# Kernel tuning notes

Hardware: AMD Instinct MI355X
Metric: run time of the kernel (lower is better)

## Reference

```python
import jax, jax.numpy as jnp
import numpy as np

CUTOFF = 5.0
NUM_RBF = 8
POLY_P = 5
AVG_NEIGH = 16.0
NUM_LAYERS = 2
NUM_RANKS = 4  # edge angular ranks 0..3 (Cartesian dims 1,3,9,27)
C = 64


def _radial(edge_vec):
    # r: [E,1]; Bessel-j0 basis with polynomial cutoff envelope (MACE-style)
    r = jnp.sqrt(jnp.sum(edge_vec * edge_vec, axis=-1, keepdims=True) + 1e-12)
    x = r / CUTOFF
    p = float(POLY_P)
    env = (1.0 - 0.5 * (p + 1.0) * (p + 2.0) * x**POLY_P
           + p * (p + 2.0) * x**(POLY_P + 1)
           - 0.5 * p * (p + 1.0) * x**(POLY_P + 2))
    env = jnp.where(x < 1.0, env, 0.0)
    k = jnp.arange(1, NUM_RBF + 1, dtype=edge_vec.dtype)
    basis = jnp.sqrt(2.0 / CUTOFF) * jnp.sin(k * jnp.pi * x) / r  # [E,K]
    return basis * env, r


def _angular(rhat):
    # Cartesian ICTD-style angular basis, ranks 0..3, norm constants sqrt(2r+1)
    E = rhat.shape[0]
    y0 = jnp.ones((E, 1), rhat.dtype)
    y1 = jnp.sqrt(3.0) * rhat  # [E,3]
    o2 = rhat[:, :, None] * rhat[:, None, :]
    y2 = jnp.sqrt(5.0) * o2.reshape(E, 9)
    o3 = o2[:, :, :, None] * rhat[:, None, None, :]
    y3 = jnp.sqrt(7.0) * o3.reshape(E, 27)
    return (y0, y1, y2, y3)


def setup_inputs() -> dict:
    key = jax.random.key(0)
    ks = jax.random.split(key, 12)
    N, E = 5000, 80000
    species = jax.random.randint(ks[0], (N,), 0, 10, dtype=jnp.int32)
    senders = jax.random.randint(ks[1], (E,), 0, N, dtype=jnp.int32)
    receivers = jax.random.randint(ks[2], (E,), 0, N, dtype=jnp.int32)
    edge_vec = 1.5 * jax.random.normal(ks[3], (E, 3), jnp.float32)
    embed_w = jax.random.normal(ks[4], (10, C), jnp.float32)
    rad_w1 = jax.random.normal(ks[5], (NUM_LAYERS, NUM_RBF, 64), jnp.float32) / np.sqrt(NUM_RBF)
    rad_w2 = jax.random.normal(ks[6], (NUM_LAYERS, 64, 64), jnp.float32) / 8.0
    rad_w3 = jax.random.normal(ks[7], (NUM_LAYERS, 64, 64), jnp.float32) / 8.0
    rad_w4 = jax.random.normal(ks[8], (NUM_LAYERS, 64, NUM_RANKS * C), jnp.float32) / 8.0
    mix_w = jax.random.normal(ks[9], (NUM_LAYERS, NUM_RANKS, C, C), jnp.float32) / 8.0
    read_w = jax.random.normal(ks[10], (NUM_LAYERS, C), jnp.float32) / 8.0
    return {"species": species, "senders": senders, "receivers": receivers,
            "edge_vec": edge_vec, "embed_w": embed_w, "rad_w1": rad_w1,
            "rad_w2": rad_w2, "rad_w3": rad_w3, "rad_w4": rad_w4,
            "mix_w": mix_w, "read_w": read_w}


def reference(species, senders, receivers, edge_vec, embed_w,
              rad_w1, rad_w2, rad_w3, rad_w4, mix_w, read_w):
    N = species.shape[0]
    E = edge_vec.shape[0]
    rb, r = _radial(edge_vec)                      # [E,K]
    rhat = edge_vec / r
    Y = _angular(rhat)                             # tuple of [E,dim_r]
    h0 = embed_w[species]                          # [N,C] species embedding
    node_energy = jnp.zeros((N,), edge_vec.dtype)
    for l in range(NUM_LAYERS):
        # radial MLP -> per-rank, per-channel edge weights [E, NUM_RANKS, C]
        h = jax.nn.silu(rb @ rad_w1[l])
        h = jax.nn.silu(h @ rad_w2[l])
        h = jax.nn.silu(h @ rad_w3[l])
        R = (h @ rad_w4[l]).reshape(E, NUM_RANKS, C)
        hj = h0[senders]                           # neighbor gather [E,C]
        h0_new = jnp.zeros_like(h0)
        for ri in range(NUM_RANKS):
            # equivariant edge tensor product: radial * scalar feat x angular
            m = (R[:, ri, :] * hj)[:, :, None] * Y[ri][:, None, :]  # [E,C,dim]
            A = jax.ops.segment_sum(m, receivers, num_segments=N) / AVG_NEIGH
            if ri == 0:
                h0_new = h0_new + A[..., 0] @ mix_w[l, 0]
            else:
                # correlation-2 invariant contraction of equivariant features
                h0_new = h0_new + jnp.einsum('ncd,ncd->nc', A, A) @ mix_w[l, ri]
        node_energy = node_energy + h0_new @ read_w[l]
        h0 = h0_new
    return node_energy
```

## Files before the change

kernel.cpp:

```cpp
#include <hip/hip_runtime.h>
#include <math.h>


#define PI_F 3.14159265358979323846f
#define LOG2E_F 1.44269504088896340736f

typedef _Float16 f16x8 __attribute__((ext_vector_type(8)));
typedef float f32x4 __attribute__((ext_vector_type(4)));

union FU { uint4 u; f16x8 h; };

__device__ __forceinline__ float silu_f(float x) {
    float e = __builtin_amdgcn_exp2f(-LOG2E_F * x);
    return x * __builtin_amdgcn_rcpf(1.0f + e);
}

__device__ __forceinline__ uint pack2_f16(float a, float b) {
    return __builtin_bit_cast(uint, __builtin_amdgcn_cvt_pkrtz(a, b));
}

__device__ __forceinline__ float unpk_f16(uint u, int hi) {
    unsigned short s = hi ? (unsigned short)(u >> 16) : (unsigned short)(u & 0xffff);
    return (float)__builtin_bit_cast(_Float16, s);
}

__global__ void k_setup(const float* __restrict__ rw1,
                        const float* __restrict__ rw2,
                        const float* __restrict__ rw3,
                        const float* __restrict__ rw4,
                        uint* __restrict__ Wf1, uint* __restrict__ Wf2,
                        uint* __restrict__ Wf3, uint* __restrict__ Wf4,
                        const int* __restrict__ species,
                        const float* __restrict__ embw,
                        float* __restrict__ h0,
                        int* __restrict__ counts, int* __restrict__ cursor,
                        int N, int NC)
{
    int tid = blockIdx.x * blockDim.x + threadIdx.x;
    if (tid < N) { counts[tid] = 0; cursor[tid] = 0; }
    if (tid < NC) {
        int n = tid >> 6, c = tid & 63;
        h0[tid] = embw[species[n]*64 + c];
    }
    if (tid < 2048) {
        int reg = tid & 3, lane = (tid >> 2) & 63, ot = (tid >> 8) & 3, l = tid >> 10;
        int out = 16*ot + (lane & 15);
        int k   = 8*(lane >> 4) + 2*reg;
        float lo = (k   < 8) ? rw1[l*512 + k*64 + out]     : 0.0f;
        float hi = (k+1 < 8) ? rw1[l*512 + (k+1)*64 + out] : 0.0f;
        Wf1[tid] = pack2_f16(lo, hi);
    }
    if (tid >= 2048 && tid < 2048 + 4096) {
        int t = tid - 2048;
        int reg = t & 3, lane = (t >> 2) & 63, kt = (t >> 8) & 1, ot = (t >> 9) & 3, l = t >> 11;
        int out = 16*ot + (lane & 15);
        int k   = 32*kt + 8*(lane >> 4) + 2*reg;
        Wf2[t] = pack2_f16(rw2[l*4096 + k*64 + out], rw2[l*4096 + (k+1)*64 + out]);
    }
    if (tid >= 6144 && tid < 6144 + 4096) {
        int t = tid - 6144;
        int reg = t & 3, lane = (t >> 2) & 63, kt = (t >> 8) & 1, ot = (t >> 9) & 3, l = t >> 11;
        int out = 16*ot + (lane & 15);
        int k   = 32*kt + 8*(lane >> 4) + 2*reg;
        Wf3[t] = pack2_f16(rw3[l*4096 + k*64 + out], rw3[l*4096 + (k+1)*64 + out]);
    }
    if (tid >= 10240 && tid < 10240 + 16384) {
        int t = tid - 10240;
        int reg = t & 3, lane = (t >> 2) & 63, kt = (t >> 8) & 1, ot = (t >> 9) & 15, l = t >> 13;
        int out = 16*ot + (lane & 15);
        int k   = 32*kt + 8*(lane >> 4) + 2*reg;
        Wf4[t] = pack2_f16(rw4[l*16384 + k*256 + out], rw4[l*16384 + (k+1)*256 + out]);
    }
}

__global__ void k_edge_basis(const float* __restrict__ ev,
                             const int* __restrict__ recv,
                             uint*  __restrict__ rbh,
                             float* __restrict__ rhat4,
                             int*   __restrict__ counts,
                             int E)
{
    int e = blockIdx.x * blockDim.x + threadIdx.x;
    if (e >= E) return;
    float vx = ev[3*e+0], vy = ev[3*e+1], vz = ev[3*e+2];
    float r2 = vx*vx + vy*vy + vz*vz + 1e-12f;
    float r  = sqrtf(r2);
    float x  = r * 0.2f;
    float x2 = x*x;
    float x5 = x2*x2*x;
    float env = 1.0f + x5*(-21.0f + x*(35.0f - 15.0f*x));
    if (x >= 1.0f) env = 0.0f;
    float pref = 0.632455532033675866f / r * env;
    float pix  = PI_F * x;
    float bas[8];
    #pragma unroll
    for (int k = 0; k < 8; ++k) bas[k] = pref * __sinf((float)(k+1) * pix);
    uint* o = rbh + (size_t)e*4;
    #pragma unroll
    for (int k = 0; k < 4; ++k) o[k] = pack2_f16(bas[2*k], bas[2*k+1]);

    float ir = 1.0f / r;
    float4 rh;
    rh.x = vx*ir; rh.y = vy*ir; rh.z = vz*ir; rh.w = 0.0f;
    *(float4*)(rhat4 + (size_t)e*4) = rh;

    atomicAdd(&counts[recv[e]], 1);
}

__global__ void k_scan(const int* __restrict__ counts, int* __restrict__ offsets, int N)
{
    __shared__ int wsum[16];
    __shared__ int basev;
    int lane = threadIdx.x & 63;
    int w    = threadIdx.x >> 6;
    if (threadIdx.x == 0) basev = 0;
    __syncthreads();
    for (int start = 0; start < N; start += 1024) {
        int i = start + (int)threadIdx.x;
        int v = (i < N) ? counts[i] : 0;
        int s = v;
        #pragma unroll
        for (int off = 1; off < 64; off <<= 1) {
            int t = __shfl_up(s, off, 64);
            if (lane >= off) s += t;
        }
        if (lane == 63) wsum[w] = s;
        __syncthreads();
        int wbase = 0;
        {
            int ws = (lane < 16) ? wsum[lane] : 0;
            #pragma unroll
            for (int off = 1; off < 16; off <<= 1) {
                int t = __shfl_up(ws, off, 64);
                if (lane >= off) ws += t;
            }
            int excl = __shfl(ws, w - 1, 64);
            wbase = (w == 0) ? 0 : excl;
        }
        if (i < N) offsets[i] = basev + wbase + s - v;
        __syncthreads();
        if (threadIdx.x == 1023) basev += wbase + s;
        __syncthreads();
    }
    if (threadIdx.x == 0) offsets[N] = basev;
}

__global__ void k_scatter(const int* __restrict__ recv,
                          const int* __restrict__ offsets,
                          int* __restrict__ cursor,
                          int* __restrict__ elist, int E)
{
    int e = blockIdx.x * blockDim.x + threadIdx.x;
    if (e >= E) return;
    int r = recv[e];
    int p = atomicAdd(&cursor[r], 1);
    elist[offsets[r] + p] = e;
}

__global__ __launch_bounds__(256) void k_sort_wave(
    const int* __restrict__ offsets, int* __restrict__ elist, int N)
{
    int lane = threadIdx.x & 63;
    int node = (blockIdx.x * blockDim.x + threadIdx.x) >> 6;
    if (node >= N) return;
    int beg = offsets[node], end = offsets[node+1];
    int d = end - beg;
    if (d <= 1) return;
    if (d <= 64) {
        int v = (lane < d) ? elist[beg + lane] : 0x7fffffff;
        int rank = 0;
        #pragma unroll 8
        for (int j = 0; j < 64; ++j) {
            int vj = __shfl(v, j, 64);
            rank += (vj < v) ? 1 : 0;
        }
        if (lane < d) elist[beg + rank] = v;
    } else {
        if (lane == 0) {
            for (int i = beg + 1; i < end; ++i) {
                int v = elist[i];
                int j = i - 1;
                while (j >= beg && elist[j] > v) { elist[j+1] = elist[j]; --j; }
                elist[j+1] = v;
            }
        }
    }
}

__global__ void k_permute(const int* __restrict__ elist,
                          const int* __restrict__ senders,
                          const float* __restrict__ rhat4,
                          int* __restrict__ eslot,
                          int* __restrict__ csr_send,
                          float* __restrict__ csr_rhat,
                          int E)
{
    int s = blockIdx.x * blockDim.x + threadIdx.x;
    if (s >= E) return;
    int e = elist[s];
    eslot[e] = s;
    csr_send[s] = senders[e];
    *(float4*)(csr_rhat + (size_t)s*4) = *(const float4*)(rhat4 + (size_t)e*4);
}

__global__ __launch_bounds__(256) void k_mlp_mfma(
    const uint* __restrict__ rbh,
    const uint* __restrict__ Wf1, const uint* __restrict__ Wf2,
    const uint* __restrict__ Wf3, const uint* __restrict__ Wf4,
    const int* __restrict__ eslot,
    uint* __restrict__ Rpk,
    int E, int tiles)
{
    __shared__ __align__(16) uint Hl[4][16][132];
    int lane = threadIdx.x & 63;
    int w    = threadIdx.x >> 6;
    int wid  = blockIdx.x * 4 + w;
    if (wid >= 2 * tiles) return;
    int l    = wid / tiles;
    int tile = wid % tiles;
    int e0   = tile * 16;

    uint (*H)[132] = Hl[w];
    int er = lane & 15;
    int kb = lane >> 4;

    f32x4 zero4 = {0.f, 0.f, 0.f, 0.f};

    FU b;
    if (kb == 0) {
        int e = e0 + er;
        if (e < E) b.u = *(const uint4*)(rbh + (size_t)e*4);
        else       b.u = make_uint4(0,0,0,0);
    } else {
        b.u = make_uint4(0,0,0,0);
    }
    f32x4 d[4];
    #pragma unroll
    for (int ot = 0; ot < 4; ++ot) {
        FU a;
        a.u = *(const uint4*)(Wf1 + ((size_t)(l*4 + ot)*64 + lane)*4);
        d[ot] = __builtin_amdgcn_mfma_f32_16x16x32_f16(a.h, b.h, zero4, 0, 0, 0);
    }
    #pragma unroll
    for (int ot = 0; ot < 4; ++ot) {
        uint p0 = pack2_f16(silu_f(d[ot][0]), silu_f(d[ot][1]));
        uint p1 = pack2_f16(silu_f(d[ot][2]), silu_f(d[ot][3]));
        uint* dst = &H[er][8*ot + 2*kb];
        dst[0] = p0; dst[1] = p1;
    }

    const uint* Wfs[2] = { Wf2, Wf3 };
    #pragma unroll
    for (int s = 0; s < 2; ++s) {
        FU hb0, hb1;
        hb0.u = *(const uint4*)&H[er][4*kb];
        hb1.u = *(const uint4*)&H[er][16 + 4*kb];
        #pragma unroll
        for (int ot = 0; ot < 4; ++ot) {
            FU a;
            a.u = *(const uint4*)(Wfs[s] + ((size_t)((l*4 + ot)*2 + 0)*64 + lane)*4);
            d[ot] = __builtin_amdgcn_mfma_f32_16x16x32_f16(a.h, hb0.h, zero4, 0, 0, 0);
            a.u = *(const uint4*)(Wfs[s] + ((size_t)((l*4 + ot)*2 + 1)*64 + lane)*4);
            d[ot] = __builtin_amdgcn_mfma_f32_16x16x32_f16(a.h, hb1.h, d[ot], 0, 0, 0);
        }
        #pragma unroll
        for (int ot = 0; ot < 4; ++ot) {
            uint p0 = pack2_f16(silu_f(d[ot][0]), silu_f(d[ot][1]));
            uint p1 = pack2_f16(silu_f(d[ot][2]), silu_f(d[ot][3]));
            uint* dst = &H[er][8*ot + 2*kb];
            dst[0] = p0; dst[1] = p1;
        }
    }

    FU hb0, hb1;
    hb0.u = *(const uint4*)&H[er][4*kb];
    hb1.u = *(const uint4*)&H[er][16 + 4*kb];
    #pragma unroll
    for (int ri = 0; ri < 4; ++ri) {
        #pragma unroll
        for (int otl = 0; otl < 4; ++otl) {
            int ot = ri*4 + otl;
            FU a;
            f32x4 d2;
            a.u = *(const uint4*)(Wf4 + ((size_t)((l*16 + ot)*2 + 0)*64 + lane)*4);
            d2 = __builtin_amdgcn_mfma_f32_16x16x32_f16(a.h, hb0.h, zero4, 0, 0, 0);
            a.u = *(const uint4*)(Wf4 + ((size_t)((l*16 + ot)*2 + 1)*64 + lane)*4);
            d2 = __builtin_amdgcn_mfma_f32_16x16x32_f16(a.h, hb1.h, d2, 0, 0, 0);
            int p = otl*8 + kb*2;
            H[er][(p  )*4 + ri] = pack2_f16(d2[0], d2[1]);
            H[er][(p+1)*4 + ri] = pack2_f16(d2[2], d2[3]);
        }
    }
    #pragma unroll
    for (int it = 0; it < 8; ++it) {
        int f   = it*64 + lane;
        int row = f >> 5;
        int q4  = (f & 31) * 4;
        int eg  = e0 + row;
        if (eg < E) {
            int slot = eslot[eg];
            *(uint4*)(Rpk + ((size_t)l*E + slot)*128 + q4) = *(const uint4*)&H[row][q4];
        }
    }
}

__global__ __launch_bounds__(256) void k_node(
    const uint*  __restrict__ Rpk,
    const float* __restrict__ h0,
    const int*   __restrict__ csr_send,
    const float* __restrict__ csr_rhat,
    const int*   __restrict__ offsets,
    const float* __restrict__ mixw,
    const float* __restrict__ readw,
    float* __restrict__ h0n,
    const float* __restrict__ eprev,
    float* __restrict__ eout,
    int N)
{
    int gtid = blockIdx.x * blockDim.x + threadIdx.x;
    int wave = gtid >> 6;
    int lane = threadIdx.x & 63;
    int w    = threadIdx.x >> 6;
    __shared__ float Bl[4][4][64];
    bool active = (wave < N);
    int n = active ? wave : 0;
    int half  = lane & 1;
    int cpair = lane >> 1;

    float a0 = 0.f;
    float a1[3]  = {0.f,0.f,0.f};
    float a2[6]  = {0.f,0.f,0.f,0.f,0.f,0.f};
    float a3[10] = {0.f,0.f,0.f,0.f,0.f,0.f,0.f,0.f,0.f,0.f};

    auto accum = [&](float x, float y, float z, float hj, uint4 qv) {
        float t0 = unpk_f16(qv.x, half) * hj;
        float t1 = unpk_f16(qv.y, half) * hj;
        float t2 = unpk_f16(qv.z, half) * hj;
        float t3 = unpk_f16(qv.w, half) * hj;
        a0 += t0;
        a1[0] = fmaf(t1, x, a1[0]);
        a1[1] = fmaf(t1, y, a1[1]);
        a1[2] = fmaf(t1, z, a1[2]);
        float qxx = x*x, qxy = x*y, qxz = x*z, qyy = y*y, qyz = y*z, qzz = z*z;
        a2[0] = fmaf(t2, qxx, a2[0]);
        a2[1] = fmaf(t2, qxy, a2[1]);
        a2[2] = fmaf(t2, qxz, a2[2]);
        a2[3] = fmaf(t2, qyy, a2[3]);
        a2[4] = fmaf(t2, qyz, a2[4]);
        a2[5] = fmaf(t2, qzz, a2[5]);
        float u0 = t3*qxx, u1 = t3*qxy, u3 = t3*qyy, u5 = t3*qzz;
        a3[0] = fmaf(u0, x, a3[0]);
        a3[1] = fmaf(u0, y, a3[1]);
        a3[2] = fmaf(u0, z, a3[2]);
        a3[3] = fmaf(u3, x, a3[3]);
        a3[4] = fmaf(u1, z, a3[4]);
        a3[5] = fmaf(u5, x, a3[5]);
        a3[6] = fmaf(u3, y, a3[6]);
        a3[7] = fmaf(u3, z, a3[7]);
        a3[8] = fmaf(u5, y, a3[8]);
        a3[9] = fmaf(u5, z, a3[9]);
    };

    if (active) {
        int beg = __builtin_amdgcn_readfirstlane(offsets[n]);
        int end = __builtin_amdgcn_readfirstlane(offsets[n+1]);
        int i = beg;
        for (; i + 4 <= end; i += 4) {
            int sn_[4]; float4 rh_[4]; float hj_[4]; uint4 q_[4];
            #pragma unroll
            for (int k = 0; k < 4; ++k) sn_[k] = csr_send[i+k];
            #pragma unroll
            for (int k = 0; k < 4; ++k) {
                rh_[k] = *(const float4*)(csr_rhat + (size_t)(i+k)*4);
                q_[k]  = *(const uint4*)(Rpk + (size_t)(i+k)*128 + cpair*4);
            }
            #pragma unroll
            for (int k = 0; k < 4; ++k) hj_[k] = h0[(size_t)sn_[k]*64 + lane];
            #pragma unroll
            for (int k = 0; k < 4; ++k)
                accum(rh_[k].x, rh_[k].y, rh_[k].z, hj_[k], q_[k]);
        }
        for (; i < end; ++i) {
            int snd = csr_send[i];
            float4 rh = *(const float4*)(csr_rhat + (size_t)i*4);
            uint4  qv = *(const uint4*)(Rpk + (size_t)i*128 + cpair*4);
            float  hj = h0[(size_t)snd*64 + lane];
            accum(rh.x, rh.y, rh.z, hj, qv);
        }
    }

    float B0 = a0 * 0.0625f;
    float s1 = a1[0]*a1[0] + a1[1]*a1[1] + a1[2]*a1[2];
    float B1 = s1 * (3.0f/256.0f);
    float s2 = a2[0]*a2[0] + a2[3]*a2[3] + a2[5]*a2[5]
             + 2.0f*(a2[1]*a2[1] + a2[2]*a2[2] + a2[4]*a2[4]);
    float B2 = s2 * (5.0f/256.0f);
    float s3 = a3[0]*a3[0] + a3[6]*a3[6] + a3[9]*a3[9]
             + 3.0f*(a3[1]*a3[1] + a3[2]*a3[2] + a3[3]*a3[3]
                   + a3[5]*a3[5] + a3[7]*a3[7] + a3[8]*a3[8])
             + 6.0f*a3[4]*a3[4];
    float B3 = s3 * (7.0f/256.0f);

    Bl[w][0][lane] = B0;
    Bl[w][1][lane] = B1;
    Bl[w][2][lane] = B2;
    Bl[w][3][lane] = B3;
    __syncthreads();

    if (active) {
        float acc = 0.0f;
        for (int ri = 0; ri < 4; ++ri) {
            #pragma unroll 8
            for (int j = 0; j < 64; ++j)
                acc = fmaf(Bl[w][ri][j], mixw[(ri*64 + j)*64 + lane], acc);
        }
        h0n[(size_t)n*64 + lane] = acc;

        float evl = acc * readw[lane];
        #pragma unroll
        for (int off = 1; off < 64; off <<= 1) evl += __shfl_xor(evl, off, 64);
        if (lane == 0) {
            float o = evl;
            if (eprev) o += eprev[n];
            eout[n] = o;
        }
    }
}

extern "C" void kernel_launch(void* const* d_in, const int* in_sizes, int n_in,
                              void* d_out, int out_size, void* d_ws, size_t ws_size,
                              hipStream_t stream)
{
    const int*   species   = (const int*)  d_in[0];
    const int*   senders   = (const int*)  d_in[1];
    const int*   receivers = (const int*)  d_in[2];
    const float* edge_vec  = (const float*)d_in[3];
    const float* embed_w   = (const float*)d_in[4];
    const float* rad_w1    = (const float*)d_in[5];
    const float* rad_w2    = (const float*)d_in[6];
    const float* rad_w3    = (const float*)d_in[7];
    const float* rad_w4    = (const float*)d_in[8];
    const float* mix_w     = (const float*)d_in[9];
    const float* read_w    = (const float*)d_in[10];

    int N = in_sizes[0];
    int E = in_sizes[1];
    float* out = (float*)d_out;

    char* ws = (char*)d_ws;
    size_t off = 0;
    auto alloc = [&](size_t bytes) -> char* {
        char* p = ws + off;
        off = (off + bytes + 255) & ~(size_t)255;
        return p;
    };
    uint*  rbh     = (uint*) alloc((size_t)E*4*sizeof(uint));
    float* rhat4   = (float*)alloc((size_t)E*4*sizeof(float));
    float* h0a     = (float*)alloc((size_t)N*64*sizeof(float));
    float* h0b     = (float*)alloc((size_t)N*64*sizeof(float));
    float* ener    = (float*)alloc((size_t)N*sizeof(float));
    int* counts    = (int*)alloc((size_t)N*sizeof(int));
    int* offsets   = (int*)alloc((size_t)(N+1)*sizeof(int));
    int* cursor    = (int*)alloc((size_t)N*sizeof(int));
    int* elist     = (int*)alloc((size_t)E*sizeof(int));
    int* eslot     = (int*)alloc((size_t)E*sizeof(int));
    int* csr_send  = (int*)alloc((size_t)E*sizeof(int));
    float* csr_rhat= (float*)alloc((size_t)E*4*sizeof(float));
    uint* Wf1      = (uint*)alloc(2048*sizeof(uint));
    uint* Wf2      = (uint*)alloc(4096*sizeof(uint));
    uint* Wf3      = (uint*)alloc(4096*sizeof(uint));
    uint* Wf4      = (uint*)alloc(16384*sizeof(uint));
    uint* Rpk      = (uint*)alloc((size_t)2*E*128*sizeof(uint));

    int NC = N * 64;
    k_setup<<<(NC + 255)/256, 256, 0, stream>>>(
        rad_w1, rad_w2, rad_w3, rad_w4, Wf1, Wf2, Wf3, Wf4,
        species, embed_w, h0a, counts, cursor, N, NC);

    k_edge_basis<<<(E + 255)/256, 256, 0, stream>>>(
        edge_vec, receivers, rbh, rhat4, counts, E);
    k_scan<<<1, 1024, 0, stream>>>(counts, offsets, N);
    k_scatter<<<(E + 255)/256, 256, 0, stream>>>(receivers, offsets, cursor, elist, E);
    k_sort_wave<<<((size_t)N*64 + 255)/256, 256, 0, stream>>>(offsets, elist, N);
    k_permute<<<(E + 255)/256, 256, 0, stream>>>(
        elist, senders, rhat4, eslot, csr_send, csr_rhat, E);

    int tiles = (E + 15) / 16;
    int waves = 2 * tiles;
    k_mlp_mfma<<<(waves + 3)/4, 256, 0, stream>>>(
        rbh, Wf1, Wf2, Wf3, Wf4, eslot, Rpk, E, tiles);

    float* hcur = h0a;
    float* hnxt = h0b;
    for (int l = 0; l < 2; ++l) {
        uint* Rl = Rpk + (size_t)l * E * 128;
        k_node<<<((size_t)N*64 + 255)/256, 256, 0, stream>>>(
            Rl, hcur, csr_send, csr_rhat, offsets,
            mix_w + (size_t)l*4*64*64,
            read_w + (size_t)l*64,
            hnxt,
            (l == 0) ? nullptr : ener,
            (l == 0) ? ener : out,
            N);
        float* tmp = hcur; hcur = hnxt; hnxt = tmp;
    }
}
```

Baseline: 113.1 us.

## Fuse sort with permute and split node edge loop across wave pairs

Merges the per-node edge sort with the CSR permutation into one kernel, so the separate permute launch and its re-read of elist go away. The node kernel now gives each node two waves that each accumulate half of the edges. Partial accumulators are combined through shared memory, and the mix-weight contraction is split by rank between the two waves. This doubles the waves working on the gather-heavy edge loop to improve latency hiding, at the cost of extra shared-memory traffic and two more block barriers.

Result: no change. 114.4 us (+1.1%).

```diff
diff --git a/kernel.cpp b/kernel.cpp
--- a/kernel.cpp
+++ b/kernel.cpp
@@ -157,15 +157,22 @@
     elist[offsets[r] + p] = e;
 }
 
-__global__ __launch_bounds__(256) void k_sort_wave(
-    const int* __restrict__ offsets, int* __restrict__ elist, int N)
+__global__ __launch_bounds__(256) void k_sort_perm(
+    const int* __restrict__ offsets,
+    int* __restrict__ elist,
+    const int* __restrict__ senders,
+    const float* __restrict__ rhat4,
+    int* __restrict__ eslot,
+    int* __restrict__ csr_send,
+    float* __restrict__ csr_rhat,
+    int N)
 {
     int lane = threadIdx.x & 63;
     int node = (blockIdx.x * blockDim.x + threadIdx.x) >> 6;
     if (node >= N) return;
     int beg = offsets[node], end = offsets[node+1];
     int d = end - beg;
-    if (d <= 1) return;
+    if (d <= 0) return;
     if (d <= 64) {
         int v = (lane < d) ? elist[beg + lane] : 0x7fffffff;
         int rank = 0;
@@ -174,7 +181,12 @@
             int vj = __shfl(v, j, 64);
             rank += (vj < v) ? 1 : 0;
         }
-        if (lane < d) elist[beg + rank] = v;
+        if (lane < d) {
+            int slot = beg + rank;
+            eslot[v] = slot;
+            csr_send[slot] = senders[v];
+            *(float4*)(csr_rhat + (size_t)slot*4) = *(const float4*)(rhat4 + (size_t)v*4);
+        }
     } else {
         if (lane == 0) {
             for (int i = beg + 1; i < end; ++i) {
@@ -183,24 +195,14 @@
                 while (j >= beg && elist[j] > v) { elist[j+1] = elist[j]; --j; }
                 elist[j+1] = v;
             }
-        }
-    }
-}
-
-__global__ void k_permute(const int* __restrict__ elist,
-                          const int* __restrict__ senders,
-                          const float* __restrict__ rhat4,
-                          int* __restrict__ eslot,
-                          int* __restrict__ csr_send,
-                          float* __restrict__ csr_rhat,
-                          int E)
-{
-    int s = blockIdx.x * blockDim.x + threadIdx.x;
-    if (s >= E) return;
-    int e = elist[s];
-    eslot[e] = s;
-    csr_send[s] = senders[e];
-    *(float4*)(csr_rhat + (size_t)s*4) = *(const float4*)(rhat4 + (size_t)e*4);
+            for (int s = beg; s < end; ++s) {
+                int e = elist[s];
+                eslot[e] = s;
+                csr_send[s] = senders[e];
+                *(float4*)(csr_rhat + (size_t)s*4) = *(const float4*)(rhat4 + (size_t)e*4);
+            }
+        }
+    }
 }
 
 __global__ __launch_bounds__(256) void k_mlp_mfma(
@@ -317,13 +319,16 @@
     float* __restrict__ eout,
     int N)
 {
-    int gtid = blockIdx.x * blockDim.x + threadIdx.x;
-    int wave = gtid >> 6;
     int lane = threadIdx.x & 63;
     int w    = threadIdx.x >> 6;
-    __shared__ float Bl[4][4][64];
-    bool active = (wave < N);
-    int n = active ? wave : 0;
+    int pair = w >> 1;
+    int sub  = w & 1;
+    int n    = blockIdx.x * 2 + pair;
+    bool active = (n < N);
+
+    __shared__ float Bp[2][20][64];
+    __shared__ float Bl[2][4][64];
+
     int half  = lane & 1;
     int cpair = lane >> 1;
 
@@ -364,8 +369,13 @@
     if (active) {
         int beg = __builtin_amdgcn_readfirstlane(offsets[n]);
         int end = __builtin_amdgcn_readfirstlane(offsets[n+1]);
-        int i = beg;
-        for (; i + 4 <= end; i += 4) {
+        int cnt = end - beg;
+        int hsz = (cnt + 1) >> 1;
+        int b0  = beg + sub * hsz;
+        int b1  = sub ? end : (beg + hsz);
+
+        int i = b0;
+        for (; i + 4 <= b1; i += 4) {
             int sn_[4]; float4 rh_[4]; float hj_[4]; uint4 q_[4];
             #pragma unroll
             for (int k = 0; k < 4; ++k) sn_[k] = csr_send[i+k];
@@ -380,7 +390,7 @@
             for (int k = 0; k < 4; ++k)
                 accum(rh_[k].x, rh_[k].y, rh_[k].z, hj_[k], q_[k]);
         }
-        for (; i < end; ++i) {
+        for (; i < b1; ++i) {
             int snd = csr_send[i];
             float4 rh = *(const float4*)(csr_rhat + (size_t)i*4);
             uint4  qv = *(const uint4*)(Rpk + (size_t)i*128 + cpair*4);
@@ -389,31 +399,59 @@
         }
     }
 
-    float B0 = a0 * 0.0625f;
-    float s1 = a1[0]*a1[0] + a1[1]*a1[1] + a1[2]*a1[2];
-    float B1 = s1 * (3.0f/256.0f);
-    float s2 = a2[0]*a2[0] + a2[3]*a2[3] + a2[5]*a2[5]
-             + 2.0f*(a2[1]*a2[1] + a2[2]*a2[2] + a2[4]*a2[4]);
-    float B2 = s2 * (5.0f/256.0f);
-    float s3 = a3[0]*a3[0] + a3[6]*a3[6] + a3[9]*a3[9]
-             + 3.0f*(a3[1]*a3[1] + a3[2]*a3[2] + a3[3]*a3[3]
-                   + a3[5]*a3[5] + a3[7]*a3[7] + a3[8]*a3[8])
-             + 6.0f*a3[4]*a3[4];
-    float B3 = s3 * (7.0f/256.0f);
-
-    Bl[w][0][lane] = B0;
-    Bl[w][1][lane] = B1;
-    Bl[w][2][lane] = B2;
-    Bl[w][3][lane] = B3;
+    if (active && sub == 1) {
+        Bp[pair][0][lane] = a0;
+        #pragma unroll
+        for (int j = 0; j < 3; ++j)  Bp[pair][1+j][lane]  = a1[j];
+        #pragma unroll
+        for (int j = 0; j < 6; ++j)  Bp[pair][4+j][lane]  = a2[j];
+        #pragma unroll
+        for (int j = 0; j < 10; ++j) Bp[pair][10+j][lane] = a3[j];
+    }
     __syncthreads();
 
+    if (active && sub == 0) {
+        a0 += Bp[pair][0][lane];
+        #pragma unroll
+        for (int j = 0; j < 3; ++j)  a1[j] += Bp[pair][1+j][lane];
+        #pragma unroll
+        for (int j = 0; j < 6; ++j)  a2[j] += Bp[pair][4+j][lane];
+        #pragma unroll
+        for (int j = 0; j < 10; ++j) a3[j] += Bp[pair][10+j][lane];
+
+        float B0 = a0 * 0.0625f;
+        float s1 = a1[0]*a1[0] + a1[1]*a1[1] + a1[2]*a1[2];
+        float B1 = s1 * (3.0f/256.0f);
+        float s2 = a2[0]*a2[0] + a2[3]*a2[3] + a2[5]*a2[5]
+                 + 2.0f*(a2[1]*a2[1] + a2[2]*a2[2] + a2[4]*a2[4]);
+        float B2 = s2 * (5.0f/256.0f);
+        float s3 = a3[0]*a3[0] + a3[6]*a3[6] + a3[9]*a3[9]
+                 + 3.0f*(a3[1]*a3[1] + a3[2]*a3[2] + a3[3]*a3[3]
+                       + a3[5]*a3[5] + a3[7]*a3[7] + a3[8]*a3[8])
+                 + 6.0f*a3[4]*a3[4];
+        float B3 = s3 * (7.0f/256.0f);
+        Bl[pair][0][lane] = B0;
+        Bl[pair][1][lane] = B1;
+        Bl[pair][2][lane] = B2;
+        Bl[pair][3][lane] = B3;
+    }
+    __syncthreads();
+
+    float accw = 0.0f;
     if (active) {
-        float acc = 0.0f;
-        for (int ri = 0; ri < 4; ++ri) {
+        #pragma unroll
+        for (int rr = 0; rr < 2; ++rr) {
+            int ri = sub*2 + rr;
             #pragma unroll 8
             for (int j = 0; j < 64; ++j)
-                acc = fmaf(Bl[w][ri][j], mixw[(ri*64 + j)*64 + lane], acc);
-        }
+                accw = fmaf(Bl[pair][ri][j], mixw[(ri*64 + j)*64 + lane], accw);
+        }
+    }
+    if (active && sub == 1) Bp[pair][0][lane] = accw;
+    __syncthreads();
+
+    if (active && sub == 0) {
+        float acc = accw + Bp[pair][0][lane];
         h0n[(size_t)n*64 + lane] = acc;
 
         float evl = acc * readw[lane];
@@ -481,9 +519,8 @@
         edge_vec, receivers, rbh, rhat4, counts, E);
     k_scan<<<1, 1024, 0, stream>>>(counts, offsets, N);
     k_scatter<<<(E + 255)/256, 256, 0, stream>>>(receivers, offsets, cursor, elist, E);
-    k_sort_wave<<<((size_t)N*64 + 255)/256, 256, 0, stream>>>(offsets, elist, N);
-    k_permute<<<(E + 255)/256, 256, 0, stream>>>(
-        elist, senders, rhat4, eslot, csr_send, csr_rhat, E);
+    k_sort_perm<<<((size_t)N*64 + 255)/256, 256, 0, stream>>>(
+        offsets, elist, senders, rhat4, eslot, csr_send, csr_rhat, N);
 
     int tiles = (E + 15) / 16;
     int waves = 2 * tiles;
@@ -494,7 +531,7 @@
     float* hnxt = h0b;
     for (int l = 0; l < 2; ++l) {
         uint* Rl = Rpk + (size_t)l * E * 128;
-        k_node<<<((size_t)N*64 + 255)/256, 256, 0, stream>>>(
+        k_node<<<(N + 1)/2, 256, 0, stream>>>(
             Rl, hcur, csr_send, csr_rhat, offsets,
             mix_w + (size_t)l*4*64*64,
             read_w + (size_t)l*64,
```

## Fuse radial MLP into per-node aggregation kernel and merge sort with permute

Applied to the files above, without the earlier changes.

Computes the edge radial MLP with MFMA inside the node aggregation kernel, in 16-edge tiles per receiver node, and reads the results from LDS. This removes the large Rpk buffer and its global write and read. Sorting and permutation of edge data (sender, rhat, radial basis) are merged into one kernel, which also drops the eslot indirection. In exchange, MLP tiles are partially empty for nodes whose degree is not a multiple of 16, which wastes MFMA work.

New measurement: 210.0 us. 85.6% more time.

```diff
diff --git a/kernel.cpp b/kernel.cpp
--- a/kernel.cpp
+++ b/kernel.cpp
@@ -157,15 +157,23 @@
     elist[offsets[r] + p] = e;
 }
 
-__global__ __launch_bounds__(256) void k_sort_wave(
-    const int* __restrict__ offsets, int* __restrict__ elist, int N)
+__global__ __launch_bounds__(256) void k_sort_perm(
+    const int* __restrict__ offsets,
+    int* __restrict__ elist,
+    const int* __restrict__ senders,
+    const float* __restrict__ rhat4,
+    const uint* __restrict__ rbh,
+    int* __restrict__ csr_send,
+    float* __restrict__ csr_rhat,
+    uint* __restrict__ csr_rbh,
+    int N)
 {
     int lane = threadIdx.x & 63;
     int node = (blockIdx.x * blockDim.x + threadIdx.x) >> 6;
     if (node >= N) return;
     int beg = offsets[node], end = offsets[node+1];
     int d = end - beg;
-    if (d <= 1) return;
+    if (d <= 0) return;
     if (d <= 64) {
         int v = (lane < d) ? elist[beg + lane] : 0x7fffffff;
         int rank = 0;
@@ -174,7 +182,12 @@
             int vj = __shfl(v, j, 64);
             rank += (vj < v) ? 1 : 0;
         }
-        if (lane < d) elist[beg + rank] = v;
+        if (lane < d) {
+            int slot = beg + rank;
+            csr_send[slot] = senders[v];
+            *(float4*)(csr_rhat + (size_t)slot*4) = *(const float4*)(rhat4 + (size_t)v*4);
+            *(uint4*)(csr_rbh + (size_t)slot*4)   = *(const uint4*)(rbh + (size_t)v*4);
+        }
     } else {
         if (lane == 0) {
             for (int i = beg + 1; i < end; ++i) {
@@ -183,129 +196,20 @@
                 while (j >= beg && elist[j] > v) { elist[j+1] = elist[j]; --j; }
                 elist[j+1] = v;
             }
-        }
-    }
-}
-
-__global__ void k_permute(const int* __restrict__ elist,
-                          const int* __restrict__ senders,
-                          const float* __restrict__ rhat4,
-                          int* __restrict__ eslot,
-                          int* __restrict__ csr_send,
-                          float* __restrict__ csr_rhat,
-                          int E)
-{
-    int s = blockIdx.x * blockDim.x + threadIdx.x;
-    if (s >= E) return;
-    int e = elist[s];
-    eslot[e] = s;
-    csr_send[s] = senders[e];
-    *(float4*)(csr_rhat + (size_t)s*4) = *(const float4*)(rhat4 + (size_t)e*4);
-}
-
-__global__ __launch_bounds__(256) void k_mlp_mfma(
-    const uint* __restrict__ rbh,
-    const uint* __restrict__ Wf1, const uint* __restrict__ Wf2,
-    const uint* __restrict__ Wf3, const uint* __restrict__ Wf4,
-    const int* __restrict__ eslot,
-    uint* __restrict__ Rpk,
-    int E, int tiles)
-{
-    __shared__ __align__(16) uint Hl[4][16][132];
-    int lane = threadIdx.x & 63;
-    int w    = threadIdx.x >> 6;
-    int wid  = blockIdx.x * 4 + w;
-    if (wid >= 2 * tiles) return;
-    int l    = wid / tiles;
-    int tile = wid % tiles;
-    int e0   = tile * 16;
-
-    uint (*H)[132] = Hl[w];
-    int er = lane & 15;
-    int kb = lane >> 4;
-
-    f32x4 zero4 = {0.f, 0.f, 0.f, 0.f};
-
-    FU b;
-    if (kb == 0) {
-        int e = e0 + er;
-        if (e < E) b.u = *(const uint4*)(rbh + (size_t)e*4);
-        else       b.u = make_uint4(0,0,0,0);
-    } else {
-        b.u = make_uint4(0,0,0,0);
-    }
-    f32x4 d[4];
-    #pragma unroll
-    for (int ot = 0; ot < 4; ++ot) {
-        FU a;
-        a.u = *(const uint4*)(Wf1 + ((size_t)(l*4 + ot)*64 + lane)*4);
-        d[ot] = __builtin_amdgcn_mfma_f32_16x16x32_f16(a.h, b.h, zero4, 0, 0, 0);
-    }
-    #pragma unroll
-    for (int ot = 0; ot < 4; ++ot) {
-        uint p0 = pack2_f16(silu_f(d[ot][0]), silu_f(d[ot][1]));
-        uint p1 = pack2_f16(silu_f(d[ot][2]), silu_f(d[ot][3]));
-        uint* dst = &H[er][8*ot + 2*kb];
-        dst[0] = p0; dst[1] = p1;
-    }
-
-    const uint* Wfs[2] = { Wf2, Wf3 };
-    #pragma unroll
-    for (int s = 0; s < 2; ++s) {
-        FU hb0, hb1;
-        hb0.u = *(const uint4*)&H[er][4*kb];
-        hb1.u = *(const uint4*)&H[er][16 + 4*kb];
-        #pragma unroll
-        for (int ot = 0; ot < 4; ++ot) {
-            FU a;
-            a.u = *(const uint4*)(Wfs[s] + ((size_t)((l*4 + ot)*2 + 0)*64 + lane)*4);
-            d[ot] = __builtin_amdgcn_mfma_f32_16x16x32_f16(a.h, hb0.h, zero4, 0, 0, 0);
-            a.u = *(const uint4*)(Wfs[s] + ((size_t)((l*4 + ot)*2 + 1)*64 + lane)*4);
-            d[ot] = __builtin_amdgcn_mfma_f32_16x16x32_f16(a.h, hb1.h, d[ot], 0, 0, 0);
-        }
-        #pragma unroll
-        for (int ot = 0; ot < 4; ++ot) {
-            uint p0 = pack2_f16(silu_f(d[ot][0]), silu_f(d[ot][1]));
-            uint p1 = pack2_f16(silu_f(d[ot][2]), silu_f(d[ot][3]));
-            uint* dst = &H[er][8*ot + 2*kb];
-            dst[0] = p0; dst[1] = p1;
-        }
-    }
-
-    FU hb0, hb1;
-    hb0.u = *(const uint4*)&H[er][4*kb];
-    hb1.u = *(const uint4*)&H[er][16 + 4*kb];
-    #pragma unroll
-    for (int ri = 0; ri < 4; ++ri) {
-        #pragma unroll
-        for (int otl = 0; otl < 4; ++otl) {
-            int ot = ri*4 + otl;
-            FU a;
-            f32x4 d2;
-            a.u = *(const uint4*)(Wf4 + ((size_t)((l*16 + ot)*2 + 0)*64 + lane)*4);
-            d2 = __builtin_amdgcn_mfma_f32_16x16x32_f16(a.h, hb0.h, zero4, 0, 0, 0);
-            a.u = *(const uint4*)(Wf4 + ((size_t)((l*16 + ot)*2 + 1)*64 + lane)*4);
-            d2 = __builtin_amdgcn_mfma_f32_16x16x32_f16(a.h, hb1.h, d2, 0, 0, 0);
-            int p = otl*8 + kb*2;
-            H[er][(p  )*4 + ri] = pack2_f16(d2[0], d2[1]);
-            H[er][(p+1)*4 + ri] = pack2_f16(d2[2], d2[3]);
-        }
-    }
-    #pragma unroll
-    for (int it = 0; it < 8; ++it) {
-        int f   = it*64 + lane;
-        int row = f >> 5;
-        int q4  = (f & 31) * 4;
-        int eg  = e0 + row;
-        if (eg < E) {
-            int slot = eslot[eg];
-            *(uint4*)(Rpk + ((size_t)l*E + slot)*128 + q4) = *(const uint4*)&H[row][q4];
-        }
-    }
-}
-
-__global__ __launch_bounds__(256) void k_node(
-    const uint*  __restrict__ Rpk,
+            for (int s = beg; s < end; ++s) {
+                int e = elist[s];
+                csr_send[s] = senders[e];
+                *(float4*)(csr_rhat + (size_t)s*4) = *(const float4*)(rhat4 + (size_t)e*4);
+                *(uint4*)(csr_rbh + (size_t)s*4)   = *(const uint4*)(rbh + (size_t)e*4);
+            }
+        }
+    }
+}
+
+__global__ __launch_bounds__(256) void k_node_fused(
+    const uint*  __restrict__ csr_rbh,
+    const uint*  __restrict__ Wf1, const uint* __restrict__ Wf2,
+    const uint*  __restrict__ Wf3, const uint* __restrict__ Wf4,
     const float* __restrict__ h0,
     const int*   __restrict__ csr_send,
     const float* __restrict__ csr_rhat,
@@ -315,17 +219,22 @@
     float* __restrict__ h0n,
     const float* __restrict__ eprev,
     float* __restrict__ eout,
-    int N)
-{
-    int gtid = blockIdx.x * blockDim.x + threadIdx.x;
-    int wave = gtid >> 6;
+    int l, int N)
+{
+    __shared__ __align__(16) uint Hl[4][16][132];
+    __shared__ float Bl[4][4][64];
     int lane = threadIdx.x & 63;
     int w    = threadIdx.x >> 6;
-    __shared__ float Bl[4][4][64];
-    bool active = (wave < N);
-    int n = active ? wave : 0;
+    int n    = blockIdx.x * 4 + w;
+    if (n >= N) return;
+
+    uint (*H)[132] = Hl[w];
+    int er = lane & 15;
+    int kb = lane >> 4;
     int half  = lane & 1;
     int cpair = lane >> 1;
+
+    f32x4 zero4 = {0.f, 0.f, 0.f, 0.f};
 
     float a0 = 0.f;
     float a1[3]  = {0.f,0.f,0.f};
@@ -361,30 +270,79 @@
         a3[9] = fmaf(u5, z, a3[9]);
     };
 
-    if (active) {
-        int beg = __builtin_amdgcn_readfirstlane(offsets[n]);
-        int end = __builtin_amdgcn_readfirstlane(offsets[n+1]);
-        int i = beg;
-        for (; i + 4 <= end; i += 4) {
-            int sn_[4]; float4 rh_[4]; float hj_[4]; uint4 q_[4];
+    int beg = __builtin_amdgcn_readfirstlane(offsets[n]);
+    int end = __builtin_amdgcn_readfirstlane(offsets[n+1]);
+
+    for (int t0 = beg; t0 < end; t0 += 16) {
+        int nt = end - t0; if (nt > 16) nt = 16;
+
+        FU b;
+        if (kb == 0 && er < nt) b.u = *(const uint4*)(csr_rbh + (size_t)(t0 + er)*4);
+        else                    b.u = make_uint4(0,0,0,0);
+        f32x4 d[4];
+        #pragma unroll
+        for (int ot = 0; ot < 4; ++ot) {
+            FU a;
+            a.u = *(const uint4*)(Wf1 + ((size_t)(l*4 + ot)*64 + lane)*4);
+            d[ot] = __builtin_amdgcn_mfma_f32_16x16x32_f16(a.h, b.h, zero4, 0, 0, 0);
+        }
+        #pragma unroll
+        for (int ot = 0; ot < 4; ++ot) {
+            uint p0 = pack2_f16(silu_f(d[ot][0]), silu_f(d[ot][1]));
+            uint p1 = pack2_f16(silu_f(d[ot][2]), silu_f(d[ot][3]));
+            uint* dst = &H[er][8*ot + 2*kb];
+            dst[0] = p0; dst[1] = p1;
+        }
+
+        const uint* Wfs[2] = { Wf2, Wf3 };
+        #pragma unroll
+        for (int s = 0; s < 2; ++s) {
+            FU hb0, hb1;
+            hb0.u = *(const uint4*)&H[er][4*kb];
+            hb1.u = *(const uint4*)&H[er][16 + 4*kb];
             #pragma unroll
-            for (int k = 0; k < 4; ++k) sn_[k] = csr_send[i+k];
+            for (int ot = 0; ot < 4; ++ot) {
+                FU a;
+                a.u = *(const uint4*)(Wfs[s] + ((size_t)((l*4 + ot)*2 + 0)*64 + lane)*4);
+                d[ot] = __builtin_amdgcn_mfma_f32_16x16x32_f16(a.h, hb0.h, zero4, 0, 0, 0);
+                a.u = *(const uint4*)(Wfs[s] + ((size_t)((l*4 + ot)*2 + 1)*64 + lane)*4);
+                d[ot] = __builtin_amdgcn_mfma_f32_16x16x32_f16(a.h, hb1.h, d[ot], 0, 0, 0);
+            }
             #pragma unroll
-            for (int k = 0; k < 4; ++k) {
-                rh_[k] = *(const float4*)(csr_rhat + (size_t)(i+k)*4);
-                q_[k]  = *(const uint4*)(Rpk + (size_t)(i+k)*128 + cpair*4);
-            }
+            for (int ot = 0; ot < 4; ++ot) {
+                uint p0 = pack2_f16(silu_f(d[ot][0]), silu_f(d[ot][1]));
+                uint p1 = pack2_f16(silu_f(d[ot][2]), silu_f(d[ot][3]));
+                uint* dst = &H[er][8*ot + 2*kb];
+                dst[0] = p0; dst[1] = p1;
+            }
+        }
+
+        FU hb0, hb1;
+        hb0.u = *(const uint4*)&H[er][4*kb];
+        hb1.u = *(const uint4*)&H[er][16 + 4*kb];
+        #pragma unroll
+        for (int ri = 0; ri < 4; ++ri) {
             #pragma unroll
-            for (int k = 0; k < 4; ++k) hj_[k] = h0[(size_t)sn_[k]*64 + lane];
-            #pragma unroll
-            for (int k = 0; k < 4; ++k)
-                accum(rh_[k].x, rh_[k].y, rh_[k].z, hj_[k], q_[k]);
-        }
-        for (; i < end; ++i) {
-            int snd = csr_send[i];
-            float4 rh = *(const float4*)(csr_rhat + (size_t)i*4);
-            uint4  qv = *(const uint4*)(Rpk + (size_t)i*128 + cpair*4);
+            for (int otl = 0; otl < 4; ++otl) {
+                int ot = ri*4 + otl;
+                FU a;
+                f32x4 d2;
+                a.u = *(const uint4*)(Wf4 + ((size_t)((l*16 + ot)*2 + 0)*64 + lane)*4);
+                d2 = __builtin_amdgcn_mfma_f32_16x16x32_f16(a.h, hb0.h, zero4, 0, 0, 0);
+                a.u = *(const uint4*)(Wf4 + ((size_t)((l*16 + ot)*2 + 1)*64 + lane)*4);
+                d2 = __builtin_amdgcn_mfma_f32_16x16x32_f16(a.h, hb1.h, d2, 0, 0, 0);
+                int p = otl*8 + kb*2;
+                H[er][(p  )*4 + ri] = pack2_f16(d2[0], d2[1]);
+                H[er][(p+1)*4 + ri] = pack2_f16(d2[2], d2[3]);
+            }
+        }
+
+        for (int j = 0; j < nt; ++j) {
+            int slot = t0 + j;
+            int snd = __builtin_amdgcn_readfirstlane(csr_send[slot]);
+            float4 rh = *(const float4*)(csr_rhat + (size_t)slot*4);
             float  hj = h0[(size_t)snd*64 + lane];
+            uint4  qv = *(const uint4*)&H[j][cpair*4];
             accum(rh.x, rh.y, rh.z, hj, qv);
         }
     }
@@ -405,25 +363,22 @@
     Bl[w][1][lane] = B1;
     Bl[w][2][lane] = B2;
     Bl[w][3][lane] = B3;
-    __syncthreads();
-
-    if (active) {
-        float acc = 0.0f;
-        for (int ri = 0; ri < 4; ++ri) {
-            #pragma unroll 8
-            for (int j = 0; j < 64; ++j)
-                acc = fmaf(Bl[w][ri][j], mixw[(ri*64 + j)*64 + lane], acc);
-        }
-        h0n[(size_t)n*64 + lane] = acc;
-
-        float evl = acc * readw[lane];
-        #pragma unroll
-        for (int off = 1; off < 64; off <<= 1) evl += __shfl_xor(evl, off, 64);
-        if (lane == 0) {
-            float o = evl;
-            if (eprev) o += eprev[n];
-            eout[n] = o;
-        }
+
+    float acc = 0.0f;
+    for (int ri = 0; ri < 4; ++ri) {
+        #pragma unroll 8
+        for (int j = 0; j < 64; ++j)
+            acc = fmaf(Bl[w][ri][j], mixw[(ri*64 + j)*64 + lane], acc);
+    }
+    h0n[(size_t)n*64 + lane] = acc;
+
+    float evl = acc * readw[lane];
+    #pragma unroll
+    for (int off = 1; off < 64; off <<= 1) evl += __shfl_xor(evl, off, 64);
+    if (lane == 0) {
+        float o = evl;
+        if (eprev) o += eprev[n];
+        eout[n] = o;
     }
 }
 
@@ -463,14 +418,13 @@
     int* offsets   = (int*)alloc((size_t)(N+1)*sizeof(int));
     int* cursor    = (int*)alloc((size_t)N*sizeof(int));
     int* elist     = (int*)alloc((size_t)E*sizeof(int));
-    int* eslot     = (int*)alloc((size_t)E*sizeof(int));
     int* csr_send  = (int*)alloc((size_t)E*sizeof(int));
     float* csr_rhat= (float*)alloc((size_t)E*4*sizeof(float));
+    uint* csr_rbh  = (uint*)alloc((size_t)E*4*sizeof(uint));
     uint* Wf1      = (uint*)alloc(2048*sizeof(uint));
     uint* Wf2      = (uint*)alloc(4096*sizeof(uint));
     uint* Wf3      = (uint*)alloc(4096*sizeof(uint));
     uint* Wf4      = (uint*)alloc(16384*sizeof(uint));
-    uint* Rpk      = (uint*)alloc((size_t)2*E*128*sizeof(uint));
 
     int NC = N * 64;
     k_setup<<<(NC + 255)/256, 256, 0, stream>>>(
@@ -481,27 +435,21 @@
         edge_vec, receivers, rbh, rhat4, counts, E);
     k_scan<<<1, 1024, 0, stream>>>(counts, offsets, N);
     k_scatter<<<(E + 255)/256, 256, 0, stream>>>(receivers, offsets, cursor, elist, E);
-    k_sort_wave<<<((size_t)N*64 + 255)/256, 256, 0, stream>>>(offsets, elist, N);
-    k_permute<<<(E + 255)/256, 256, 0, stream>>>(
-        elist, senders, rhat4, eslot, csr_send, csr_rhat, E);
-
-    int tiles = (E + 15) / 16;
-    int waves = 2 * tiles;
-    k_mlp_mfma<<<(waves + 3)/4, 256, 0, stream>>>(
-        rbh, Wf1, Wf2, Wf3, Wf4, eslot, Rpk, E, tiles);
+    k_sort_perm<<<((size_t)N*64 + 255)/256, 256, 0, stream>>>(
+        offsets, elist, senders, rhat4, rbh, csr_send, csr_rhat, csr_rbh, N);
 
     float* hcur = h0a;
     float* hnxt = h0b;
     for (int l = 0; l < 2; ++l) {
-        uint* Rl = Rpk + (size_t)l * E * 128;
-        k_node<<<((size_t)N*64 + 255)/256, 256, 0, stream>>>(
-            Rl, hcur, csr_send, csr_rhat, offsets,
+        k_node_fused<<<(N + 3)/4, 256, 0, stream>>>(
+            csr_rbh, Wf1, Wf2, Wf3, Wf4,
+            hcur, csr_send, csr_rhat, offsets,
             mix_w + (size_t)l*4*64*64,
             read_w + (size_t)l*64,
             hnxt,
             (l == 0) ? nullptr : ener,
             (l == 0) ? ener : out,
-            N);
+            l, N);
         float* tmp = hcur; hcur = hnxt; hnxt = tmp;
     }
 }
```

## Fuse edge sort with CSR permutation and double MLP tile per wave

Applied to the files above, without the earlier changes.

Merges the per-node edge sort with the permutation kernel, so each lane writes eslot, csr_send and csr_rhat straight from its computed rank and one launch plus one elist pass go away. The MLP kernel now processes 32 edges per wave instead of 16, reusing each loaded weight fragment across two MFMA tiles, with 2 waves per 128-thread block. This halves global weight-fragment loads per edge but raises register pressure and cuts the number of waves in flight.

Result: no change. 112.9 us (-0.2%).

```diff
diff --git a/kernel.cpp b/kernel.cpp
--- a/kernel.cpp
+++ b/kernel.cpp
@@ -157,15 +157,22 @@
     elist[offsets[r] + p] = e;
 }
 
-__global__ __launch_bounds__(256) void k_sort_wave(
-    const int* __restrict__ offsets, int* __restrict__ elist, int N)
+__global__ __launch_bounds__(256) void k_sort_perm(
+    const int* __restrict__ offsets,
+    int* __restrict__ elist,
+    const int* __restrict__ senders,
+    const float* __restrict__ rhat4,
+    int* __restrict__ eslot,
+    int* __restrict__ csr_send,
+    float* __restrict__ csr_rhat,
+    int N)
 {
     int lane = threadIdx.x & 63;
     int node = (blockIdx.x * blockDim.x + threadIdx.x) >> 6;
     if (node >= N) return;
     int beg = offsets[node], end = offsets[node+1];
     int d = end - beg;
-    if (d <= 1) return;
+    if (d <= 0) return;
     if (d <= 64) {
         int v = (lane < d) ? elist[beg + lane] : 0x7fffffff;
         int rank = 0;
@@ -174,7 +181,12 @@
             int vj = __shfl(v, j, 64);
             rank += (vj < v) ? 1 : 0;
         }
-        if (lane < d) elist[beg + rank] = v;
+        if (lane < d) {
+            int slot = beg + rank;
+            eslot[v] = slot;
+            csr_send[slot] = senders[v];
+            *(float4*)(csr_rhat + (size_t)slot*4) = *(const float4*)(rhat4 + (size_t)v*4);
+        }
     } else {
         if (lane == 0) {
             for (int i = beg + 1; i < end; ++i) {
@@ -183,27 +195,17 @@
                 while (j >= beg && elist[j] > v) { elist[j+1] = elist[j]; --j; }
                 elist[j+1] = v;
             }
-        }
-    }
-}
-
-__global__ void k_permute(const int* __restrict__ elist,
-                          const int* __restrict__ senders,
-                          const float* __restrict__ rhat4,
-                          int* __restrict__ eslot,
-                          int* __restrict__ csr_send,
-                          float* __restrict__ csr_rhat,
-                          int E)
-{
-    int s = blockIdx.x * blockDim.x + threadIdx.x;
-    if (s >= E) return;
-    int e = elist[s];
-    eslot[e] = s;
-    csr_send[s] = senders[e];
-    *(float4*)(csr_rhat + (size_t)s*4) = *(const float4*)(rhat4 + (size_t)e*4);
-}
-
-__global__ __launch_bounds__(256) void k_mlp_mfma(
+            for (int s = beg; s < end; ++s) {
+                int e = elist[s];
+                eslot[e] = s;
+                csr_send[s] = senders[e];
+                *(float4*)(csr_rhat + (size_t)s*4) = *(const float4*)(rhat4 + (size_t)e*4);
+            }
+        }
+    }
+}
+
+__global__ __launch_bounds__(128) void k_mlp_mfma(
     const uint* __restrict__ rbh,
     const uint* __restrict__ Wf1, const uint* __restrict__ Wf2,
     const uint* __restrict__ Wf3, const uint* __restrict__ Wf4,
@@ -211,14 +213,14 @@
     uint* __restrict__ Rpk,
     int E, int tiles)
 {
-    __shared__ __align__(16) uint Hl[4][16][132];
+    __shared__ __align__(16) uint Hl[2][32][132];
     int lane = threadIdx.x & 63;
     int w    = threadIdx.x >> 6;
-    int wid  = blockIdx.x * 4 + w;
+    int wid  = blockIdx.x * 2 + w;
     if (wid >= 2 * tiles) return;
     int l    = wid / tiles;
     int tile = wid % tiles;
-    int e0   = tile * 16;
+    int e0   = tile * 32;
 
     uint (*H)[132] = Hl[w];
     int er = lane & 15;
@@ -226,73 +228,88 @@
 
     f32x4 zero4 = {0.f, 0.f, 0.f, 0.f};
 
-    FU b;
+    FU b0, b1;
+    b0.u = make_uint4(0,0,0,0);
+    b1.u = make_uint4(0,0,0,0);
     if (kb == 0) {
-        int e = e0 + er;
-        if (e < E) b.u = *(const uint4*)(rbh + (size_t)e*4);
-        else       b.u = make_uint4(0,0,0,0);
-    } else {
-        b.u = make_uint4(0,0,0,0);
-    }
-    f32x4 d[4];
+        int ea = e0 + er, eb = e0 + 16 + er;
+        if (ea < E) b0.u = *(const uint4*)(rbh + (size_t)ea*4);
+        if (eb < E) b1.u = *(const uint4*)(rbh + (size_t)eb*4);
+    }
+    f32x4 d0[4], d1[4];
     #pragma unroll
     for (int ot = 0; ot < 4; ++ot) {
         FU a;
         a.u = *(const uint4*)(Wf1 + ((size_t)(l*4 + ot)*64 + lane)*4);
-        d[ot] = __builtin_amdgcn_mfma_f32_16x16x32_f16(a.h, b.h, zero4, 0, 0, 0);
+        d0[ot] = __builtin_amdgcn_mfma_f32_16x16x32_f16(a.h, b0.h, zero4, 0, 0, 0);
+        d1[ot] = __builtin_amdgcn_mfma_f32_16x16x32_f16(a.h, b1.h, zero4, 0, 0, 0);
     }
     #pragma unroll
     for (int ot = 0; ot < 4; ++ot) {
-        uint p0 = pack2_f16(silu_f(d[ot][0]), silu_f(d[ot][1]));
-        uint p1 = pack2_f16(silu_f(d[ot][2]), silu_f(d[ot][3]));
-        uint* dst = &H[er][8*ot + 2*kb];
-        dst[0] = p0; dst[1] = p1;
+        uint* dA = &H[er][8*ot + 2*kb];
+        dA[0] = pack2_f16(silu_f(d0[ot][0]), silu_f(d0[ot][1]));
+        dA[1] = pack2_f16(silu_f(d0[ot][2]), silu_f(d0[ot][3]));
+        uint* dB = &H[16 + er][8*ot + 2*kb];
+        dB[0] = pack2_f16(silu_f(d1[ot][0]), silu_f(d1[ot][1]));
+        dB[1] = pack2_f16(silu_f(d1[ot][2]), silu_f(d1[ot][3]));
     }
 
     const uint* Wfs[2] = { Wf2, Wf3 };
     #pragma unroll
     for (int s = 0; s < 2; ++s) {
-        FU hb0, hb1;
-        hb0.u = *(const uint4*)&H[er][4*kb];
-        hb1.u = *(const uint4*)&H[er][16 + 4*kb];
+        FU hA0, hA1, hB0, hB1;
+        hA0.u = *(const uint4*)&H[er][4*kb];
+        hA1.u = *(const uint4*)&H[er][16 + 4*kb];
+        hB0.u = *(const uint4*)&H[16 + er][4*kb];
+        hB1.u = *(const uint4*)&H[16 + er][16 + 4*kb];
         #pragma unroll
         for (int ot = 0; ot < 4; ++ot) {
             FU a;
             a.u = *(const uint4*)(Wfs[s] + ((size_t)((l*4 + ot)*2 + 0)*64 + lane)*4);
-            d[ot] = __builtin_amdgcn_mfma_f32_16x16x32_f16(a.h, hb0.h, zero4, 0, 0, 0);
+            d0[ot] = __builtin_amdgcn_mfma_f32_16x16x32_f16(a.h, hA0.h, zero4, 0, 0, 0);
+            d1[ot] = __builtin_amdgcn_mfma_f32_16x16x32_f16(a.h, hB0.h, zero4, 0, 0, 0);
             a.u = *(const uint4*)(Wfs[s] + ((size_t)((l*4 + ot)*2 + 1)*64 + lane)*4);
-            d[ot] = __builtin_amdgcn_mfma_f32_16x16x32_f16(a.h, hb1.h, d[ot], 0, 0, 0);
+            d0[ot] = __builtin_amdgcn_mfma_f32_16x16x32_f16(a.h, hA1.h, d0[ot], 0, 0, 0);
+            d1[ot] = __builtin_amdgcn_mfma_f32_16x16x32_f16(a.h, hB1.h, d1[ot], 0, 0, 0);
         }
         #pragma unroll
         for (int ot = 0; ot < 4; ++ot) {
-            uint p0 = pack2_f16(silu_f(d[ot][0]), silu_f(d[ot][1]));
-            uint p1 = pack2_f16(silu_f(d[ot][2]), silu_f(d[ot][3]));
-            uint* dst = &H[er][8*ot + 2*kb];
-            dst[0] = p0; dst[1] = p1;
-        }
-    }
-
-    FU hb0, hb1;
-    hb0.u = *(const uint4*)&H[er][4*kb];
-    hb1.u = *(const uint4*)&H[er][16 + 4*kb];
+            uint* dA = &H[er][8*ot + 2*kb];
+            dA[0] = pack2_f16(silu_f(d0[ot][0]), silu_f(d0[ot][1]));
+            dA[1] = pack2_f16(silu_f(d0[ot][2]), silu_f(d0[ot][3]));
+            uint* dB = &H[16 + er][8*ot + 2*kb];
+            dB[0] = pack2_f16(silu_f(d1[ot][0]), silu_f(d1[ot][1]));
+            dB[1] = pack2_f16(silu_f(d1[ot][2]), silu_f(d1[ot][3]));
+        }
+    }
+
+    FU hA0, hA1, hB0, hB1;
+    hA0.u = *(const uint4*)&H[er][4*kb];
+    hA1.u = *(const uint4*)&H[er][16 + 4*kb];
+    hB0.u = *(const uint4*)&H[16 + er][4*kb];
+    hB1.u = *(const uint4*)&H[16 + er][16 + 4*kb];
     #pragma unroll
     for (int ri = 0; ri < 4; ++ri) {
         #pragma unroll
         for (int otl = 0; otl < 4; ++otl) {
             int ot = ri*4 + otl;
             FU a;
-            f32x4 d2;
+            f32x4 dA, dB;
             a.u = *(const uint4*)(Wf4 + ((size_t)((l*16 + ot)*2 + 0)*64 + lane)*4);
-            d2 = __builtin_amdgcn_mfma_f32_16x16x32_f16(a.h, hb0.h, zero4, 0, 0, 0);
+            dA = __builtin_amdgcn_mfma_f32_16x16x32_f16(a.h, hA0.h, zero4, 0, 0, 0);
+            dB = __builtin_amdgcn_mfma_f32_16x16x32_f16(a.h, hB0.h, zero4, 0, 0, 0);
             a.u = *(const uint4*)(Wf4 + ((size_t)((l*16 + ot)*2 + 1)*64 + lane)*4);
-            d2 = __builtin_amdgcn_mfma_f32_16x16x32_f16(a.h, hb1.h, d2, 0, 0, 0);
+            dA = __builtin_amdgcn_mfma_f32_16x16x32_f16(a.h, hA1.h, dA, 0, 0, 0);
+            dB = __builtin_amdgcn_mfma_f32_16x16x32_f16(a.h, hB1.h, dB, 0, 0, 0);
             int p = otl*8 + kb*2;
-            H[er][(p  )*4 + ri] = pack2_f16(d2[0], d2[1]);
-            H[er][(p+1)*4 + ri] = pack2_f16(d2[2], d2[3]);
-        }
-    }
-    #pragma unroll
-    for (int it = 0; it < 8; ++it) {
+            H[er][(p  )*4 + ri] = pack2_f16(dA[0], dA[1]);
+            H[er][(p+1)*4 + ri] = pack2_f16(dA[2], dA[3]);
+            H[16 + er][(p  )*4 + ri] = pack2_f16(dB[0], dB[1]);
+            H[16 + er][(p+1)*4 + ri] = pack2_f16(dB[2], dB[3]);
+        }
+    }
+    #pragma unroll
+    for (int it = 0; it < 16; ++it) {
         int f   = it*64 + lane;
         int row = f >> 5;
         int q4  = (f & 31) * 4;
@@ -481,13 +498,12 @@
         edge_vec, receivers, rbh, rhat4, counts, E);
     k_scan<<<1, 1024, 0, stream>>>(counts, offsets, N);
     k_scatter<<<(E + 255)/256, 256, 0, stream>>>(receivers, offsets, cursor, elist, E);
-    k_sort_wave<<<((size_t)N*64 + 255)/256, 256, 0, stream>>>(offsets, elist, N);
-    k_permute<<<(E + 255)/256, 256, 0, stream>>>(
-        elist, senders, rhat4, eslot, csr_send, csr_rhat, E);
-
-    int tiles = (E + 15) / 16;
+    k_sort_perm<<<((size_t)N*64 + 255)/256, 256, 0, stream>>>(
+        offsets, elist, senders, rhat4, eslot, csr_send, csr_rhat, N);
+
+    int tiles = (E + 31) / 32;
     int waves = 2 * tiles;
-    k_mlp_mfma<<<(waves + 3)/4, 256, 0, stream>>>(
+    k_mlp_mfma<<<(waves + 1)/2, 128, 0, stream>>>(
         rbh, Wf1, Wf2, Wf3, Wf4, eslot, Rpk, E, tiles);
 
     float* hcur = h0a;
```
